# Performance work log

Hardware: AMD Instinct MI355X
Metric: run time of the kernel (lower is better)

Reference implementation:

```python
import jax, jax.numpy as jnp
import numpy as np

N_NODES = 100000
N_EDGES = 1600000
NFEAT = 128
NHID = 128
NS = 64
NCLASS = 16
B = 8192


def setup_inputs() -> dict:
    key = jax.random.key(0)
    ks = jax.random.split(key, 12)
    s = jax.random.normal(ks[0], (B, NS), dtype=jnp.float32)
    x = jax.random.normal(ks[1], (N_NODES, NFEAT), dtype=jnp.float32)
    row = jax.random.randint(ks[2], (N_EDGES,), 0, N_NODES)
    col = jax.random.randint(ks[3], (N_EDGES,), 0, N_NODES)
    val = jax.random.uniform(ks[4], (N_EDGES,), dtype=jnp.float32)
    index = jax.random.randint(ks[5], (B,), 0, N_NODES)
    # learned parameters (glorot-ish scale)
    W1 = jax.random.normal(ks[6], (NFEAT, NHID), dtype=jnp.float32) / np.sqrt(NFEAT)
    b1 = jnp.zeros((NHID,), dtype=jnp.float32)
    W2 = jax.random.normal(ks[7], (NHID, NHID), dtype=jnp.float32) / np.sqrt(NHID)
    b2 = jnp.zeros((NHID,), dtype=jnp.float32)
    Wl = jax.random.normal(ks[8], (NHID + NS, NCLASS), dtype=jnp.float32) / np.sqrt(NHID + NS)
    bl = jnp.zeros((NCLASS,), dtype=jnp.float32)
    return {"s": s, "x": x, "row": row, "col": col, "val": val,
            "index": index, "W1": W1, "b1": b1, "W2": W2, "b2": b2,
            "Wl": Wl, "bl": bl}


def reference(s, x, row, col, val, index, W1, b1, W2, b2, Wl, bl):
    n = x.shape[0]

    def spmm(h):
        # adj @ h with adj in COO form: out[r] += val_e * h[c]
        return jax.ops.segment_sum(val[:, None] * h[col], row, num_segments=n)

    # dropout is identity in eval mode (training=False)
    h = jax.nn.relu(spmm(x @ W1) + b1)          # gc1 + relu
    h = spmm(h @ W2) + b2                        # gc2
    z = jnp.concatenate([h[index], s], axis=1) @ Wl + bl  # [B, nclass]
    return jax.nn.log_softmax(z, axis=1)
```

## Files before the change

kernel.cpp:

```cpp
#include <hip/hip_runtime.h>
#include <math.h>

#define N_NODES 100000
#define N_EDGES 1600000
#define NFEAT 128
#define NHID 128
#define NS 64
#define NCLASS 16
#define BB 8192

#define B1_SHIFT 11
#define NB1 49
#define SUB_SHIFT 5
#define NSUB 3125
#define CHUNK 1024
#define HWG 256
#define BINC_CAP 2048

typedef unsigned long long ull;
typedef unsigned int uint;


__device__ __forceinline__ unsigned short f2bf(float f) {
  unsigned int u = __float_as_uint(f);
  return (unsigned short)((u + 0x7fffu + ((u >> 16) & 1u)) >> 16);
}
__device__ __forceinline__ float bflo(unsigned int u) {
  return __uint_as_float(u << 16);
}
__device__ __forceinline__ float bfhi(unsigned int u) {
  return __uint_as_float(u & 0xffff0000u);
}
__device__ __forceinline__ unsigned int packbf2(float lo, float hi) {
  return (unsigned int)f2bf(lo) | ((unsigned int)f2bf(hi) << 16);
}


__device__ __forceinline__ ull pack_edge(float v, int r, int c) {
  return ((ull)(__float_as_uint(v) >> 2) << 34) | ((ull)(unsigned)r << 17) | (unsigned)c;
}
__device__ __forceinline__ int edge_col(ull p) { return (int)(p & 0x1FFFFu); }
__device__ __forceinline__ int edge_row(ull p) { return (int)((unsigned)(p >> 17) & 0x1FFFFu); }
__device__ __forceinline__ float edge_val(ull p) {
  return __uint_as_float(((unsigned)(p >> 34)) << 2);
}


__global__ __launch_bounds__(256) void histsub_kernel(const int* __restrict__ row,
                                                      int* __restrict__ subcnt) {
  __shared__ int lh[NSUB];
  int tid = threadIdx.x;
  for (int i = tid; i < NSUB; i += 256) lh[i] = 0;
  __syncthreads();
  for (long i = (long)blockIdx.x * 256 + tid; i < N_EDGES; i += (long)HWG * 256)
    atomicAdd(&lh[row[i] >> SUB_SHIFT], 1);
  __syncthreads();
  for (int i = tid; i < NSUB; i += 256) {
    int c = lh[i];
    if (c) atomicAdd(&subcnt[i], c);
  }
}


__global__ __launch_bounds__(1024) void scanall_kernel(const int* __restrict__ subcnt,
                                                       int* __restrict__ sub_offs,
                                                       int* __restrict__ gcur1,
                                                       int* __restrict__ gcur2) {
  __shared__ int sd[1024];
  int tid = threadIdx.x;
  int b0 = tid * 4;
  int vv[4];
  int loc = 0;
#pragma unroll
  for (int k = 0; k < 4; ++k) {
    int i = b0 + k;
    vv[k] = (i < NSUB) ? subcnt[i] : 0;
    loc += vv[k];
  }
  sd[tid] = loc;
  __syncthreads();
  for (int o = 1; o < 1024; o <<= 1) {
    int add = (tid >= o) ? sd[tid - o] : 0;
    __syncthreads();
    sd[tid] += add;
    __syncthreads();
  }
  int pre = sd[tid] - loc;
#pragma unroll
  for (int k = 0; k < 4; ++k) {
    int i = b0 + k;
    if (i < NSUB) {
      sub_offs[i] = pre;
      gcur2[i] = pre;
      if ((i & 63) == 0) gcur1[i >> 6] = pre;
      pre += vv[k];
    }
  }
  if (tid == 1023) sub_offs[NSUB] = sd[1023];
}


__global__ __launch_bounds__(256) void binA_kernel(const int* __restrict__ row,
                                                   const int* __restrict__ col,
                                                   const float* __restrict__ val,
                                                   int* __restrict__ gcur1,
                                                   ull* __restrict__ ebuf1) {
  __shared__ ull stage[CHUNK];
  __shared__ int hist[NB1], lofs[NB1 + 1], lcur[NB1], gbase[NB1];
  int tid = threadIdx.x;
  for (long base = (long)blockIdx.x * CHUNK; base < N_EDGES; base += (long)gridDim.x * CHUNK) {
    int cnt = (int)min((long)CHUNK, (long)N_EDGES - base);
    if (tid < NB1) hist[tid] = 0;
    __syncthreads();
    ull e[4]; int bk[4];
#pragma unroll
    for (int v = 0; v < 4; ++v) {
      int i = v * 256 + tid;
      bk[v] = -1;
      if (i < cnt) {
        long g = base + i;
        int r = row[g];
        e[v] = pack_edge(val[g], r, col[g]);
        bk[v] = r >> B1_SHIFT;
        atomicAdd(&hist[bk[v]], 1);
      }
    }
    __syncthreads();
    if (tid < 64) {
      int h = (tid < NB1) ? hist[tid] : 0;
      int x = h;
      for (int o = 1; o < 64; o <<= 1) {
        int y = __shfl_up(x, o);
        if (tid >= o) x += y;
      }
      if (tid < NB1) { lofs[tid] = x - h; lcur[tid] = x - h; }
      if (tid == 63) lofs[NB1] = x;
    }
    __syncthreads();
#pragma unroll
    for (int v = 0; v < 4; ++v) {
      if (bk[v] >= 0) {
        int pos = atomicAdd(&lcur[bk[v]], 1);
        stage[pos] = e[v];
      }
    }
    __syncthreads();
    if (tid < NB1) {
      int h = hist[tid];
      if (h > 0) gbase[tid] = atomicAdd(&gcur1[tid], h);
    }
    __syncthreads();
    for (int s = tid; s < cnt; s += 256) {
      int lo = 0, hi = NB1;
      while (hi - lo > 1) {
        int mid = (lo + hi) >> 1;
        if (lofs[mid] <= s) lo = mid; else hi = mid;
      }
      ebuf1[gbase[lo] + (s - lofs[lo])] = stage[s];
    }
    __syncthreads();
  }
}


__global__ __launch_bounds__(256) void binB_kernel(const ull* __restrict__ ebuf1,
                                                   const int* __restrict__ sub_offs,
                                                   int* __restrict__ gcur2,
                                                   ull* __restrict__ edat) {
  __shared__ ull stage[CHUNK];
  __shared__ int hist[64], lofs[65], lcur[64], gbase[64];
  int tid = threadIdx.x;
  int b1 = blockIdx.x >> 3, w = blockIdx.x & 7;
  int rbeg = sub_offs[b1 << 6];
  int rend = sub_offs[min((b1 + 1) << 6, NSUB)];
  for (int base = rbeg + w * CHUNK; base < rend; base += 8 * CHUNK) {
    int cnt = min(CHUNK, rend - base);
    if (tid < 64) hist[tid] = 0;
    __syncthreads();
    ull e[4]; int bk[4];
#pragma unroll
    for (int v = 0; v < 4; ++v) {
      int i = v * 256 + tid;
      bk[v] = -1;
      if (i < cnt) {
        e[v] = ebuf1[base + i];
        bk[v] = (edge_row(e[v]) >> SUB_SHIFT) - (b1 << 6);
        atomicAdd(&hist[bk[v]], 1);
      }
    }
    __syncthreads();
    if (tid < 64) {
      int h = hist[tid];
      int x = h;
      for (int o = 1; o < 64; o <<= 1) {
        int y = __shfl_up(x, o);
        if (tid >= o) x += y;
      }
      lofs[tid] = x - h;
      lcur[tid] = x - h;
      if (tid == 63) lofs[64] = x;
    }
    __syncthreads();
#pragma unroll
    for (int v = 0; v < 4; ++v) {
      if (bk[v] >= 0) {
        int pos = atomicAdd(&lcur[bk[v]], 1);
        stage[pos] = e[v];
      }
    }
    __syncthreads();
    if (tid < 64) {
      int h = hist[tid];
      if (h > 0) gbase[tid] = atomicAdd(&gcur2[(b1 << 6) + tid], h);
    }
    __syncthreads();
    for (int s = tid; s < cnt; s += 256) {
      int lo = 0, hi = 64;
      while (hi - lo > 1) {
        int mid = (lo + hi) >> 1;
        if (lofs[mid] <= s) lo = mid; else hi = mid;
      }
      edat[gbase[lo] + (s - lofs[lo])] = stage[s];
    }
    __syncthreads();
  }
}


__global__ __launch_bounds__(256) void binC_kernel(const int* __restrict__ sub_offs,
                                                   ull* __restrict__ edat,
                                                   ull* __restrict__ ebuf1,
                                                   int* __restrict__ offs) {
  __shared__ ull es[BINC_CAP];
  __shared__ int rcnt[32], rcur[32];
  int s = blockIdx.x, tid = threadIdx.x;
  int r0 = s << SUB_SHIFT;
  int beg = sub_offs[s], end = sub_offs[s + 1];
  int n = end - beg;
  if (tid < 32) rcnt[tid] = 0;
  __syncthreads();
  if (n <= BINC_CAP) {
    for (int i = tid; i < n; i += 256) {
      ull p = edat[beg + i];
      es[i] = p;
      atomicAdd(&rcnt[edge_row(p) & 31], 1);
    }
    __syncthreads();
    if (tid < 32) {
      int h = rcnt[tid];
      int x = h;
      for (int o = 1; o < 32; o <<= 1) {
        int y = __shfl_up(x, o, 32);
        if (tid >= o) x += y;
      }
      rcur[tid] = x - h;
      offs[r0 + tid] = beg + x - h;
      if (s == NSUB - 1 && tid == 31) offs[N_NODES] = end;
    }
    __syncthreads();
    for (int i = tid; i < n; i += 256) {
      ull p = es[i];
      int pos = atomicAdd(&rcur[edge_row(p) & 31], 1);
      edat[beg + pos] = p;
    }
  } else {
    for (int i = tid; i < n; i += 256) {
      ull p = edat[beg + i];
      ebuf1[beg + i] = p;
      atomicAdd(&rcnt[edge_row(p) & 31], 1);
    }
    __syncthreads();
    if (tid < 32) {
      int h = rcnt[tid];
      int x = h;
      for (int o = 1; o < 32; o <<= 1) {
        int y = __shfl_up(x, o, 32);
        if (tid >= o) x += y;
      }
      rcur[tid] = x - h;
      offs[r0 + tid] = beg + x - h;
      if (s == NSUB - 1 && tid == 31) offs[N_NODES] = end;
    }
    __syncthreads();
    for (int i = tid; i < n; i += 256) {
      ull p = ebuf1[beg + i];
      int pos = atomicAdd(&rcur[edge_row(p) & 31], 1);
      edat[beg + pos] = p;
    }
  }
}


__global__ __launch_bounds__(256) void mask_kernel(const int* __restrict__ offs,
                                                   const ull* __restrict__ edat,
                                                   const int* __restrict__ index,
                                                   int* __restrict__ flag) {
  int t = blockIdx.x * 256 + threadIdx.x;
  int r = index[t];
  int s = offs[r], e = offs[r + 1];
  for (int j = s; j < e; ++j) flag[edge_col(edat[j])] = 1;
}


__global__ __launch_bounds__(256) void wconv2_kernel(const float* __restrict__ W1,
                                                     const float* __restrict__ W2,
                                                     uint* __restrict__ Wt1,
                                                     uint* __restrict__ Wt2) {
  int blk = blockIdx.x;
  const float* W = (blk < 32) ? W1 : W2;
  uint* Wt = (blk < 32) ? Wt1 : Wt2;
  int idx = (blk & 31) * 256 + threadIdx.x;
  int n = idx >> 6, kc = idx & 63;
  float lo = W[(2 * kc) * 128 + n];
  float hi = W[(2 * kc + 1) * 128 + n];
  Wt[idx] = packbf2(lo, hi);
}


typedef __attribute__((ext_vector_type(8))) __bf16 bf16x8;
typedef __attribute__((ext_vector_type(4))) float f32x4;
union FragU { uint4 u; bf16x8 b; };

#define LDSTR 68

template <int OUT_BF16>
__global__ __launch_bounds__(256) void mfma_gemm_kernel(const float* __restrict__ A,
                                                        const uint* __restrict__ Wt_g,
                                                        const float* __restrict__ bias,
                                                        void* __restrict__ C,
                                                        int nrows) {
  __shared__ uint As_s[64 * LDSTR];
  __shared__ uint Wt_s[128 * LDSTR];
  int tid = threadIdx.x;
  int rbase = blockIdx.x * 64;

  {
    const uint2* src = (const uint2*)Wt_g;
#pragma unroll
    for (int i = 0; i < 16; ++i) {
      int j = i * 256 + tid;
      int n = j >> 5, c2 = (j & 31) * 2;
      uint2 v = src[j];
      Wt_s[n * LDSTR + c2] = v.x;
      Wt_s[n * LDSTR + c2 + 1] = v.y;
    }
  }
  {
    const float4* src = (const float4*)(A + (long)rbase * 128);
#pragma unroll
    for (int i = 0; i < 8; ++i) {
      int f = i * 256 + tid;
      int m = f >> 5;
      float4 v = (rbase + m < nrows) ? src[f] : make_float4(0.f, 0.f, 0.f, 0.f);
      int c = (f & 31) * 2;
      As_s[m * LDSTR + c]     = packbf2(v.x, v.y);
      As_s[m * LDSTR + c + 1] = packbf2(v.z, v.w);
    }
  }
  __syncthreads();

  int w = tid >> 6, lane = tid & 63;
  int quad = lane >> 4, lr = lane & 15;
  int n0 = w * 32;

  f32x4 acc[4][2];
#pragma unroll
  for (int mt = 0; mt < 4; ++mt)
#pragma unroll
    for (int nt = 0; nt < 2; ++nt) acc[mt][nt] = (f32x4){0.f, 0.f, 0.f, 0.f};

#pragma unroll
  for (int kk = 0; kk < 4; ++kk) {
    int kc = kk * 16 + quad * 4;
    FragU fb0, fb1;
    fb0.u = *(const uint4*)&Wt_s[(n0 + lr) * LDSTR + kc];
    fb1.u = *(const uint4*)&Wt_s[(n0 + 16 + lr) * LDSTR + kc];
#pragma unroll
    for (int mt = 0; mt < 4; ++mt) {
      FragU fa;
      fa.u = *(const uint4*)&As_s[(mt * 16 + lr) * LDSTR + kc];
      acc[mt][0] = __builtin_amdgcn_mfma_f32_16x16x32_bf16(fa.b, fb0.b, acc[mt][0], 0, 0, 0);
      acc[mt][1] = __builtin_amdgcn_mfma_f32_16x16x32_bf16(fa.b, fb1.b, acc[mt][1], 0, 0, 0);
    }
  }

#pragma unroll
  for (int mt = 0; mt < 4; ++mt) {
#pragma unroll
    for (int nt = 0; nt < 2; ++nt) {
      int col = n0 + nt * 16 + lr;
      float bv = OUT_BF16 ? 0.f : bias[col];
#pragma unroll
      for (int r = 0; r < 4; ++r) {
        int row = rbase + mt * 16 + quad * 4 + r;
        if (row < nrows) {
          if (OUT_BF16)
            ((unsigned short*)C)[(long)row * 128 + col] = f2bf(acc[mt][nt][r]);
          else
            ((float*)C)[(long)row * 128 + col] = acc[mt][nt][r] + bv;
        }
      }
    }
  }
}


__device__ __forceinline__ void fma_row(float* acc, float v, uint4 u) {
  acc[0] = fmaf(v, bflo(u.x), acc[0]);
  acc[1] = fmaf(v, bfhi(u.x), acc[1]);
  acc[2] = fmaf(v, bflo(u.y), acc[2]);
  acc[3] = fmaf(v, bfhi(u.y), acc[3]);
  acc[4] = fmaf(v, bflo(u.z), acc[4]);
  acc[5] = fmaf(v, bfhi(u.z), acc[5]);
  acc[6] = fmaf(v, bflo(u.w), acc[6]);
  acc[7] = fmaf(v, bfhi(u.w), acc[7]);
}

__global__ __launch_bounds__(256) void spmm_row_kernel(const int* __restrict__ offs,
                                                       const ull* __restrict__ edat,
                                                       const unsigned short* __restrict__ a,
                                                       const float* __restrict__ bias,
                                                       unsigned short* __restrict__ h,
                                                       const int* __restrict__ flag) {
  int wave = threadIdx.x >> 6;
  int lane = threadIdx.x & 63;
  int r = blockIdx.x * 4 + wave;
  if (!flag[r]) return;
  int g = lane >> 4, l = lane & 15;
  int s = offs[r], e = offs[r + 1];
  float acc[8] = {0.f, 0.f, 0.f, 0.f, 0.f, 0.f, 0.f, 0.f};
  int j = s + g;
  for (; j + 4 < e; j += 8) {
    ull p0 = edat[j];
    ull p1 = edat[j + 4];
    uint4 u0 = *(const uint4*)(a + (long)edge_col(p0) * 128 + l * 8);
    uint4 u1 = *(const uint4*)(a + (long)edge_col(p1) * 128 + l * 8);
    fma_row(acc, edge_val(p0), u0);
    fma_row(acc, edge_val(p1), u1);
  }
  if (j < e) {
    ull p = edat[j];
    uint4 u = *(const uint4*)(a + (long)edge_col(p) * 128 + l * 8);
    fma_row(acc, edge_val(p), u);
  }
#pragma unroll
  for (int k = 0; k < 8; ++k) {
    acc[k] += __shfl_xor(acc[k], 16);
    acc[k] += __shfl_xor(acc[k], 32);
  }
  if (g == 0) {
    float4 b0 = *(const float4*)(bias + l * 8);
    float4 b1 = *(const float4*)(bias + l * 8 + 4);
    uint4 o;
    o.x = packbf2(fmaxf(acc[0] + b0.x, 0.f), fmaxf(acc[1] + b0.y, 0.f));
    o.y = packbf2(fmaxf(acc[2] + b0.z, 0.f), fmaxf(acc[3] + b0.w, 0.f));
    o.z = packbf2(fmaxf(acc[4] + b1.x, 0.f), fmaxf(acc[5] + b1.y, 0.f));
    o.w = packbf2(fmaxf(acc[6] + b1.z, 0.f), fmaxf(acc[7] + b1.w, 0.f));
    *(uint4*)(h + (long)r * 128 + l * 8) = o;
  }
}

__global__ __launch_bounds__(256) void spmm_sel_kernel(const int* __restrict__ offs,
                                                       const ull* __restrict__ edat,
                                                       const unsigned short* __restrict__ h1,
                                                       const int* __restrict__ index,
                                                       float* __restrict__ g2) {
  int wave = threadIdx.x >> 6;
  int lane = threadIdx.x & 63;
  int b = blockIdx.x * 4 + wave;
  int g = lane >> 4, l = lane & 15;
  int r = index[b];
  int s = offs[r], e = offs[r + 1];
  float acc[8] = {0.f, 0.f, 0.f, 0.f, 0.f, 0.f, 0.f, 0.f};
  int j = s + g;
  for (; j + 4 < e; j += 8) {
    ull p0 = edat[j];
    ull p1 = edat[j + 4];
    uint4 u0 = *(const uint4*)(h1 + (long)edge_col(p0) * 128 + l * 8);
    uint4 u1 = *(const uint4*)(h1 + (long)edge_col(p1) * 128 + l * 8);
    fma_row(acc, edge_val(p0), u0);
    fma_row(acc, edge_val(p1), u1);
  }
  if (j < e) {
    ull p = edat[j];
    uint4 u = *(const uint4*)(h1 + (long)edge_col(p) * 128 + l * 8);
    fma_row(acc, edge_val(p), u);
  }
#pragma unroll
  for (int k = 0; k < 8; ++k) {
    acc[k] += __shfl_xor(acc[k], 16);
    acc[k] += __shfl_xor(acc[k], 32);
  }
  if (g == 0) {
    float* op = g2 + (long)b * 128 + l * 8;
    *(float4*)(op + 0) = make_float4(acc[0], acc[1], acc[2], acc[3]);
    *(float4*)(op + 4) = make_float4(acc[4], acc[5], acc[6], acc[7]);
  }
}


__global__ __launch_bounds__(128) void final_kernel(const float* __restrict__ t,
                                                    const float* __restrict__ s,
                                                    const float* __restrict__ Wl,
                                                    const float* __restrict__ bl,
                                                    float* __restrict__ out) {
  int b = blockIdx.x * 128 + threadIdx.x;
  float z[16];
#pragma unroll
  for (int c = 0; c < 16; ++c) z[c] = bl[c];
  const float4* tb = (const float4*)(t + (long)b * 128);
#pragma unroll 4
  for (int k4 = 0; k4 < 32; ++k4) {
    float4 tv = tb[k4];
    const float* w = Wl + (k4 * 4) * 16;
#pragma unroll
    for (int c = 0; c < 16; ++c)
      z[c] += tv.x * w[c] + tv.y * w[16 + c] + tv.z * w[32 + c] + tv.w * w[48 + c];
  }
  const float4* sb = (const float4*)(s + (long)b * 64);
#pragma unroll 4
  for (int k4 = 0; k4 < 16; ++k4) {
    float4 sv = sb[k4];
    const float* w = Wl + (128 + k4 * 4) * 16;
#pragma unroll
    for (int c = 0; c < 16; ++c)
      z[c] += sv.x * w[c] + sv.y * w[16 + c] + sv.z * w[32 + c] + sv.w * w[48 + c];
  }
  float m = z[0];
#pragma unroll
  for (int c = 1; c < 16; ++c) m = fmaxf(m, z[c]);
  float sum = 0.f;
#pragma unroll
  for (int c = 0; c < 16; ++c) sum += expf(z[c] - m);
  float lse = m + logf(sum);
  float* ob = out + (long)b * 16;
#pragma unroll
  for (int c = 0; c < 16; ++c) ob[c] = z[c] - lse;
}


extern "C" void kernel_launch(void* const* d_in, const int* in_sizes, int n_in,
                              void* d_out, int out_size, void* d_ws, size_t ws_size,
                              hipStream_t stream) {
  const float* s_in  = (const float*)d_in[0];
  const float* x     = (const float*)d_in[1];
  const int*   row   = (const int*)d_in[2];
  const int*   col   = (const int*)d_in[3];
  const float* val   = (const float*)d_in[4];
  const int*   index = (const int*)d_in[5];
  const float* W1    = (const float*)d_in[6];
  const float* b1    = (const float*)d_in[7];
  const float* W2    = (const float*)d_in[8];
  const float* b2    = (const float*)d_in[9];
  const float* Wl    = (const float*)d_in[10];
  const float* bl    = (const float*)d_in[11];
  float* out = (float*)d_out;

  ull* edat  = (ull*)d_ws;
  ull* ebuf1 = edat + N_EDGES;
  unsigned short* a  = (unsigned short*)(ebuf1 + N_EDGES);
  unsigned short* h1 = a + (size_t)N_NODES * 128;
  float* g2   = (float*)(h1 + (size_t)N_NODES * 128);
  float* tmat = g2 + (size_t)BB * 128;
  int* flag   = (int*)(tmat + (size_t)BB * 128);
  int* subcnt = flag + N_NODES;
  int* offs   = subcnt + NSUB;
  int* sub_offs = offs + (N_NODES + 1);
  int* gcur1  = sub_offs + (NSUB + 1);
  int* gcur2  = gcur1 + NB1;
  uint* Wt1   = (uint*)(gcur2 + NSUB);
  uint* Wt2   = Wt1 + 8192;

  hipMemsetAsync(flag, 0, (N_NODES + NSUB) * sizeof(int), stream);

  histsub_kernel<<<HWG, 256, 0, stream>>>(row, subcnt);
  scanall_kernel<<<1, 1024, 0, stream>>>(subcnt, sub_offs, gcur1, gcur2);

  binA_kernel<<<512, 256, 0, stream>>>(row, col, val, gcur1, ebuf1);
  binB_kernel<<<NB1 * 8, 256, 0, stream>>>(ebuf1, sub_offs, gcur2, edat);
  binC_kernel<<<NSUB, 256, 0, stream>>>(sub_offs, edat, ebuf1, offs);
  mask_kernel<<<BB / 256, 256, 0, stream>>>(offs, edat, index, flag);

  wconv2_kernel<<<64, 256, 0, stream>>>(W1, W2, Wt1, Wt2);

  mfma_gemm_kernel<1><<<(N_NODES + 63) / 64, 256, 0, stream>>>(x, Wt1, nullptr, a, N_NODES);
  spmm_row_kernel<<<N_NODES / 4, 256, 0, stream>>>(offs, edat, a, b1, h1, flag);
  spmm_sel_kernel<<<BB / 4, 256, 0, stream>>>(offs, edat, h1, index, g2);
  mfma_gemm_kernel<0><<<BB / 64, 256, 0, stream>>>(g2, Wt2, b2, tmat, BB);
  final_kernel<<<BB / 128, 128, 0, stream>>>(tmat, s_in, Wl, bl, out);
}
```

Baseline: 318.3 us.

## Prune edges to needed rows before binning and replace bucket binary search

Before sorting, the code now builds a mask of the selected output rows and of their neighbour columns with one pass over the raw COO edges. This replaces the old post-sort mask kernel. The mask is packed into a per-row keep bitmap. Histogram and binA then drop edges whose row is never needed, so sorting and SpMM handle fewer edges. binA/binB also take larger chunks of 2048 and store each staged edge's bucket id in shared memory instead of binary-searching offsets. The trade-off is an extra edge pass with random reads of `sel` and scattered `flag` writes, plus more shared memory per block, which may lower occupancy.

```diff
diff --git a/kernel.cpp b/kernel.cpp
--- a/kernel.cpp
+++ b/kernel.cpp
@@ -13,7 +13,7 @@
 #define NB1 49
 #define SUB_SHIFT 5
 #define NSUB 3125
-#define CHUNK 1024
+#define CHUNKA 2048
 #define HWG 256
 #define BINC_CAP 2048
 
@@ -46,14 +46,49 @@
 }
 
 
+__global__ __launch_bounds__(256) void selbuild_kernel(const int* __restrict__ index,
+                                                       int* __restrict__ sel) {
+  int t = blockIdx.x * 256 + threadIdx.x;
+  sel[index[t]] = 1;
+}
+
+__global__ __launch_bounds__(256) void selflag_kernel(const int* __restrict__ row,
+                                                      const int* __restrict__ col,
+                                                      const int* __restrict__ sel,
+                                                      int* __restrict__ flag) {
+  int i = blockIdx.x * blockDim.x + threadIdx.x;
+  int stride = gridDim.x * blockDim.x;
+  for (; i < N_EDGES; i += stride)
+    if (sel[row[i]]) flag[col[i]] = 1;
+}
+
+__global__ __launch_bounds__(256) void keepbits_kernel(const int* __restrict__ flag,
+                                                       const int* __restrict__ sel,
+                                                       uint* __restrict__ keepbits) {
+  int t = blockIdx.x * 256 + threadIdx.x;
+  if (t >= NSUB) return;
+  uint w = 0;
+  int base = t * 32;
+#pragma unroll
+  for (int k = 0; k < 32; ++k) {
+    int r = base + k;
+    if (r < N_NODES && (flag[r] | sel[r])) w |= (1u << k);
+  }
+  keepbits[t] = w;
+}
+
+
 __global__ __launch_bounds__(256) void histsub_kernel(const int* __restrict__ row,
+                                                      const uint* __restrict__ keepbits,
                                                       int* __restrict__ subcnt) {
   __shared__ int lh[NSUB];
   int tid = threadIdx.x;
   for (int i = tid; i < NSUB; i += 256) lh[i] = 0;
   __syncthreads();
-  for (long i = (long)blockIdx.x * 256 + tid; i < N_EDGES; i += (long)HWG * 256)
-    atomicAdd(&lh[row[i] >> SUB_SHIFT], 1);
+  for (long i = (long)blockIdx.x * 256 + tid; i < N_EDGES; i += (long)HWG * 256) {
+    int r = row[i];
+    if ((keepbits[r >> 5] >> (r & 31)) & 1u) atomicAdd(&lh[r >> SUB_SHIFT], 1);
+  }
   __syncthreads();
   for (int i = tid; i < NSUB; i += 256) {
     int c = lh[i];
@@ -103,26 +138,30 @@
 __global__ __launch_bounds__(256) void binA_kernel(const int* __restrict__ row,
                                                    const int* __restrict__ col,
                                                    const float* __restrict__ val,
+                                                   const uint* __restrict__ keepbits,
                                                    int* __restrict__ gcur1,
                                                    ull* __restrict__ ebuf1) {
-  __shared__ ull stage[CHUNK];
+  __shared__ ull stage[CHUNKA];
+  __shared__ short bkt[CHUNKA];
   __shared__ int hist[NB1], lofs[NB1 + 1], lcur[NB1], gbase[NB1];
   int tid = threadIdx.x;
-  for (long base = (long)blockIdx.x * CHUNK; base < N_EDGES; base += (long)gridDim.x * CHUNK) {
-    int cnt = (int)min((long)CHUNK, (long)N_EDGES - base);
+  for (long base = (long)blockIdx.x * CHUNKA; base < N_EDGES; base += (long)gridDim.x * CHUNKA) {
+    int cnt = (int)min((long)CHUNKA, (long)N_EDGES - base);
     if (tid < NB1) hist[tid] = 0;
     __syncthreads();
-    ull e[4]; int bk[4];
-#pragma unroll
-    for (int v = 0; v < 4; ++v) {
+    ull e[8]; int bk[8];
+#pragma unroll
+    for (int v = 0; v < 8; ++v) {
       int i = v * 256 + tid;
       bk[v] = -1;
       if (i < cnt) {
         long g = base + i;
         int r = row[g];
-        e[v] = pack_edge(val[g], r, col[g]);
-        bk[v] = r >> B1_SHIFT;
-        atomicAdd(&hist[bk[v]], 1);
+        if ((keepbits[r >> 5] >> (r & 31)) & 1u) {
+          e[v] = pack_edge(val[g], r, col[g]);
+          bk[v] = r >> B1_SHIFT;
+          atomicAdd(&hist[bk[v]], 1);
+        }
       }
     }
     __syncthreads();
@@ -138,10 +177,11 @@
     }
     __syncthreads();
 #pragma unroll
-    for (int v = 0; v < 4; ++v) {
+    for (int v = 0; v < 8; ++v) {
       if (bk[v] >= 0) {
         int pos = atomicAdd(&lcur[bk[v]], 1);
         stage[pos] = e[v];
+        bkt[pos] = (short)bk[v];
       }
     }
     __syncthreads();
@@ -150,12 +190,9 @@
       if (h > 0) gbase[tid] = atomicAdd(&gcur1[tid], h);
     }
     __syncthreads();
-    for (int s = tid; s < cnt; s += 256) {
-      int lo = 0, hi = NB1;
-      while (hi - lo > 1) {
-        int mid = (lo + hi) >> 1;
-        if (lofs[mid] <= s) lo = mid; else hi = mid;
-      }
+    int tot = lofs[NB1];
+    for (int s = tid; s < tot; s += 256) {
+      int lo = bkt[s];
       ebuf1[gbase[lo] + (s - lofs[lo])] = stage[s];
     }
     __syncthreads();
@@ -167,19 +204,20 @@
                                                    const int* __restrict__ sub_offs,
                                                    int* __restrict__ gcur2,
                                                    ull* __restrict__ edat) {
-  __shared__ ull stage[CHUNK];
+  __shared__ ull stage[CHUNKA];
+  __shared__ short bkt[CHUNKA];
   __shared__ int hist[64], lofs[65], lcur[64], gbase[64];
   int tid = threadIdx.x;
   int b1 = blockIdx.x >> 3, w = blockIdx.x & 7;
   int rbeg = sub_offs[b1 << 6];
   int rend = sub_offs[min((b1 + 1) << 6, NSUB)];
-  for (int base = rbeg + w * CHUNK; base < rend; base += 8 * CHUNK) {
-    int cnt = min(CHUNK, rend - base);
+  for (int base = rbeg + w * CHUNKA; base < rend; base += 8 * CHUNKA) {
+    int cnt = min(CHUNKA, rend - base);
     if (tid < 64) hist[tid] = 0;
     __syncthreads();
-    ull e[4]; int bk[4];
-#pragma unroll
-    for (int v = 0; v < 4; ++v) {
+    ull e[8]; int bk[8];
+#pragma unroll
+    for (int v = 0; v < 8; ++v) {
       int i = v * 256 + tid;
       bk[v] = -1;
       if (i < cnt) {
@@ -202,10 +240,11 @@
     }
     __syncthreads();
 #pragma unroll
-    for (int v = 0; v < 4; ++v) {
+    for (int v = 0; v < 8; ++v) {
       if (bk[v] >= 0) {
         int pos = atomicAdd(&lcur[bk[v]], 1);
         stage[pos] = e[v];
+        bkt[pos] = (short)bk[v];
       }
     }
     __syncthreads();
@@ -215,11 +254,7 @@
     }
     __syncthreads();
     for (int s = tid; s < cnt; s += 256) {
-      int lo = 0, hi = 64;
-      while (hi - lo > 1) {
-        int mid = (lo + hi) >> 1;
-        if (lofs[mid] <= s) lo = mid; else hi = mid;
-      }
+      int lo = bkt[s];
       edat[gbase[lo] + (s - lofs[lo])] = stage[s];
     }
     __syncthreads();
@@ -288,17 +323,6 @@
       edat[beg + pos] = p;
     }
   }
-}
-
-
-__global__ __launch_bounds__(256) void mask_kernel(const int* __restrict__ offs,
-                                                   const ull* __restrict__ edat,
-                                                   const int* __restrict__ index,
-                                                   int* __restrict__ flag) {
-  int t = blockIdx.x * 256 + threadIdx.x;
-  int r = index[t];
-  int s = offs[r], e = offs[r + 1];
-  for (int j = s; j < e; ++j) flag[edge_col(edat[j])] = 1;
 }
 
 
@@ -563,23 +587,28 @@
   float* g2   = (float*)(h1 + (size_t)N_NODES * 128);
   float* tmat = g2 + (size_t)BB * 128;
   int* flag   = (int*)(tmat + (size_t)BB * 128);
-  int* subcnt = flag + N_NODES;
+  int* sel    = flag + N_NODES;
+  int* subcnt = sel + N_NODES;
   int* offs   = subcnt + NSUB;
   int* sub_offs = offs + (N_NODES + 1);
   int* gcur1  = sub_offs + (NSUB + 1);
   int* gcur2  = gcur1 + NB1;
-  uint* Wt1   = (uint*)(gcur2 + NSUB);
+  uint* keepbits = (uint*)(gcur2 + NSUB);
+  uint* Wt1   = keepbits + NSUB;
   uint* Wt2   = Wt1 + 8192;
 
-  hipMemsetAsync(flag, 0, (N_NODES + NSUB) * sizeof(int), stream);
-
-  histsub_kernel<<<HWG, 256, 0, stream>>>(row, subcnt);
+  hipMemsetAsync(flag, 0, (2 * N_NODES + NSUB) * sizeof(int), stream);
+
+  selbuild_kernel<<<BB / 256, 256, 0, stream>>>(index, sel);
+  selflag_kernel<<<4096, 256, 0, stream>>>(row, col, sel, flag);
+  keepbits_kernel<<<(NSUB + 255) / 256, 256, 0, stream>>>(flag, sel, keepbits);
+
+  histsub_kernel<<<HWG, 256, 0, stream>>>(row, keepbits, subcnt);
   scanall_kernel<<<1, 1024, 0, stream>>>(subcnt, sub_offs, gcur1, gcur2);
 
-  binA_kernel<<<512, 256, 0, stream>>>(row, col, val, gcur1, ebuf1);
+  binA_kernel<<<512, 256, 0, stream>>>(row, col, val, keepbits, gcur1, ebuf1);
   binB_kernel<<<NB1 * 8, 256, 0, stream>>>(ebuf1, sub_offs, gcur2, edat);
   binC_kernel<<<NSUB, 256, 0, stream>>>(sub_offs, edat, ebuf1, offs);
-  mask_kernel<<<BB / 256, 256, 0, stream>>>(offs, edat, index, flag);
 
   wconv2_kernel<<<64, 256, 0, stream>>>(W1, W2, Wt1, Wt2);
 
```

After: 307.1 us. 1.04x faster.
